# Kernel tuning notes

Hardware: AMD Instinct MI355X
Metric: run time of the kernel (lower is better)

Reference implementation:

```python
import jax, jax.numpy as jnp
import numpy as np

E = 1024
H = 16
NUM_WEIGHTS = 9


def setup_inputs() -> dict:
    key = jax.random.key(0)
    ks = jax.random.split(key, 5)
    T, B = 1024, 4
    x = jax.random.normal(ks[0], (T, B, E), dtype=jnp.float32)
    # xavier-uniform-ish init scales
    w_in = jax.random.uniform(ks[1], (NUM_WEIGHTS * E, E), dtype=jnp.float32,
                              minval=-1.0, maxval=1.0) * np.sqrt(6.0 / (NUM_WEIGHTS * E + E))
    b_in = jnp.zeros((NUM_WEIGHTS * E,), dtype=jnp.float32)
    w_out = jax.random.uniform(ks[2], (E, E), dtype=jnp.float32,
                               minval=-1.0, maxval=1.0) * np.sqrt(6.0 / (E + E))
    b_out = jnp.zeros((E,), dtype=jnp.float32)
    return {"x": x, "w_in": w_in, "b_in": b_in, "w_out": w_out, "b_out": b_out}


def _heads(t, T, B, hd):
    # [T, B, E] -> [B*H, T, hd]
    return t.reshape(T, B * H, hd).transpose(1, 0, 2)


def reference(x, w_in, b_in, w_out, b_out):
    T, B, _ = x.shape
    hd = E // H
    scaling = hd ** -0.5
    gumbel_alpha = 1.0  # const_gumbel_alpha path

    proj = jnp.einsum('tbe,fe->tbf', x, w_in) + b_in  # [T, B, 9E]
    (q, k, v, q_left, k_left, q_right, k_right,
     q_local, k_local) = jnp.split(proj, NUM_WEIGHTS, axis=-1)

    q = q * scaling
    q_local = q_local * scaling

    q, k, v = _heads(q, T, B, hd), _heads(k, T, B, hd), _heads(v, T, B, hd)
    q_left, k_left = _heads(q_left, T, B, hd), _heads(k_left, T, B, hd)
    q_right, k_right = _heads(q_right, T, B, hd), _heads(k_right, T, B, hd)
    q_local, k_local = _heads(q_local, T, B, hd), _heads(k_local, T, B, hd)

    # --- prepare_local_masking (no padding mask) ---
    left_w = jnp.einsum('btd,bsd->bts', q_left, k_left)    # [BH, T, S]
    right_w = jnp.einsum('btd,bsd->bts', q_right, k_right)
    left_sm = jax.nn.softmax(gumbel_alpha * left_w, axis=-1)
    right_sm = jax.nn.softmax(gumbel_alpha * right_w, axis=-1)

    triu = jnp.triu(jnp.ones((T, T), dtype=x.dtype))       # [S, S]
    triu_t = triu.T
    # compute_lrmask2localmask
    left_mask = left_sm @ triu
    right_mask = right_sm @ triu_t
    bw_left_mask = left_sm @ triu_t
    bw_right_mask = right_sm @ triu
    local_mask = left_mask * right_mask + bw_left_mask * bw_right_mask  # [BH, T, S]

    # --- global attention branch ---
    global_w = jnp.einsum('btd,bsd->bts', q, k)
    global_probs = jax.nn.softmax(global_w, axis=-1)

    # --- local attention branch, gated by differentiable-window mask ---
    local_w = jnp.einsum('btd,bsd->bts', q_local, k_local)
    local_sm = jax.nn.softmax(local_w, axis=-1)
    masked_local = local_sm * local_mask
    local_probs = masked_local / masked_local.sum(axis=-1, keepdims=True)

    attn_probs = 0.5 * (global_probs + local_probs)
    attn = jnp.einsum('bts,bsd->btd', attn_probs, v)        # [BH, T, hd]
    attn = attn.transpose(1, 0, 2).reshape(T, B, E)
    out = jnp.einsum('tbe,fe->tbf', attn, w_out) + b_out
    return out
```

## Files before the change

### kernel.cpp

```cpp
#include <hip/hip_runtime.h>
#include <math.h>


typedef _Float16 half8 __attribute__((ext_vector_type(8)));
typedef _Float16 half4v __attribute__((ext_vector_type(4)));
typedef _Float16 half2v __attribute__((ext_vector_type(2)));
typedef float f32x4 __attribute__((ext_vector_type(4)));

#define MFMA16(A, B, C) __builtin_amdgcn_mfma_f32_16x16x32_f16(A, B, C, 0, 0, 0)

#define SMEM_ATTN ((1088 + 10240 + 256 * 65) * 4)

static __device__ __forceinline__ unsigned packhl(_Float16 a, _Float16 b) {
  half2v v; v[0] = a; v[1] = b;
  return __builtin_bit_cast(unsigned, v);
}

__global__ __launch_bounds__(256)
void split_hl(const float* __restrict__ x, _Float16* __restrict__ xh,
              _Float16* __restrict__ xl) {
  const int i = blockIdx.x * 256 + threadIdx.x;
  const float4 v = ((const float4*)x)[i];
  half4v h, l;
  const float* f = (const float*)&v;
#pragma unroll
  for (int e = 0; e < 4; ++e) {
    h[e] = (_Float16)f[e];
    l[e] = (_Float16)(f[e] - (float)h[e]);
  }
  ((half4v*)xh)[i] = h;
  ((half4v*)xl)[i] = l;
}

template<int MODE>
__global__ __launch_bounds__(256, 2)
void gemm_mfma(const float* __restrict__ A, const float* __restrict__ B,
               const float* __restrict__ bias, float* __restrict__ C,
               _Float16* __restrict__ Ph, _Float16* __restrict__ Pl,
               const _Float16* __restrict__ Axh, const _Float16* __restrict__ Axl,
               int M, int N, int K) {
  __shared__ _Float16 Ah[128 * 64], Al[128 * 64], Bh[128 * 64], Bl[128 * 64];
  const int tid = threadIdx.x;
  const int m0 = blockIdx.x * 128, n0 = blockIdx.y * 128;
  const int wave = tid >> 6, lane = tid & 63;
  const int g2 = lane >> 4, c = lane & 15;
  const int wm = (wave >> 1) * 64, wn = (wave & 1) * 64;

  const int srow = tid >> 1;
  const int shalf = (tid & 1) * 32;
  const int swz = (srow & 7) << 3;
  const float* ap = A + (size_t)(m0 + srow) * K + shalf;
  const float* bp = B + (size_t)(n0 + srow) * K + shalf;
  const _Float16* aph = Axh + (size_t)(m0 + srow) * K + shalf;
  const _Float16* apl = Axl + (size_t)(m0 + srow) * K + shalf;

  f32x4 acc[4][4];
#pragma unroll
  for (int i = 0; i < 4; ++i)
#pragma unroll
    for (int j = 0; j < 4; ++j) acc[i][j] = (f32x4){0.f, 0.f, 0.f, 0.f};

  for (int k0 = 0; k0 < K; k0 += 64) {
    float4 av[8], bv[8];
    half8 ah8[4], al8[4];
    if (MODE == 1) {
#pragma unroll
      for (int u = 0; u < 4; ++u) {
        ah8[u] = *(const half8*)(aph + k0 + u * 8);
        al8[u] = *(const half8*)(apl + k0 + u * 8);
      }
    } else {
#pragma unroll
      for (int u = 0; u < 8; ++u) av[u] = *(const float4*)(ap + k0 + u * 4);
    }
#pragma unroll
    for (int u = 0; u < 8; ++u) bv[u] = *(const float4*)(bp + k0 + u * 4);
    __syncthreads();
    if (MODE == 1) {
#pragma unroll
      for (int u = 0; u < 4; ++u) {
        const int cc = (shalf + u * 8) ^ swz;
        *(half8*)&Ah[srow * 64 + cc] = ah8[u];
        *(half8*)&Al[srow * 64 + cc] = al8[u];
      }
    }
#pragma unroll
    for (int u = 0; u < 8; ++u) {
      const int cc = (shalf + u * 4) ^ swz;
      half4v h4b, l4b;
      const float* fb = (const float*)&bv[u];
#pragma unroll
      for (int e = 0; e < 4; ++e) {
        _Float16 hb = (_Float16)fb[e];
        h4b[e] = hb; l4b[e] = (_Float16)(fb[e] - (float)hb);
      }
      if (MODE == 0) {
        half4v h4a, l4a;
        const float* fa = (const float*)&av[u];
#pragma unroll
        for (int e = 0; e < 4; ++e) {
          _Float16 ha = (_Float16)fa[e];
          h4a[e] = ha; l4a[e] = (_Float16)(fa[e] - (float)ha);
        }
        *(half4v*)&Ah[srow * 64 + cc] = h4a;
        *(half4v*)&Al[srow * 64 + cc] = l4a;
      }
      *(half4v*)&Bh[srow * 64 + cc] = h4b;
      *(half4v*)&Bl[srow * 64 + cc] = l4b;
    }
    __syncthreads();
#pragma unroll
    for (int ks = 0; ks < 2; ++ks) {
      const int kb = ks * 32 + 8 * g2;
      half8 a_h[4], a_l[4];
#pragma unroll
      for (int i = 0; i < 4; ++i) {
        const int row = wm + i * 16 + c;
        const int cc = kb ^ ((row & 7) << 3);
        a_h[i] = *(const half8*)&Ah[row * 64 + cc];
        a_l[i] = *(const half8*)&Al[row * 64 + cc];
      }
#pragma unroll
      for (int j = 0; j < 4; ++j) {
        const int rowb = wn + j * 16 + c;
        const int cc = kb ^ ((rowb & 7) << 3);
        const half8 b_h = *(const half8*)&Bh[rowb * 64 + cc];
        const half8 b_l = *(const half8*)&Bl[rowb * 64 + cc];
#pragma unroll
        for (int i = 0; i < 4; ++i) {
          acc[i][j] = MFMA16(a_h[i], b_h, acc[i][j]);
          acc[i][j] = MFMA16(a_h[i], b_l, acc[i][j]);
          acc[i][j] = MFMA16(a_l[i], b_h, acc[i][j]);
        }
      }
    }
  }

#pragma unroll
  for (int j = 0; j < 4; ++j) {
    const int nj = n0 + wn + j * 16 + c;
    const float bz = bias[nj];
    if (MODE == 0) {
#pragma unroll
      for (int i = 0; i < 4; ++i)
#pragma unroll
        for (int q = 0; q < 4; ++q) {
          const int mi = m0 + wm + i * 16 + 4 * g2 + q;
          C[(size_t)mi * N + nj] = acc[i][j][q] + bz;
        }
    } else {
      const int w = nj >> 10, hh = (nj >> 6) & 15, d = nj & 63;
      const float scale = (w == 0 || w == 7) ? 0.125f : 1.0f;
#pragma unroll
      for (int i = 0; i < 4; ++i)
#pragma unroll
        for (int q = 0; q < 4; ++q) {
          const int mi = m0 + wm + i * 16 + 4 * g2 + q;
          const int t = mi >> 2, b2 = mi & 3;
          const size_t bb = ((size_t)w * 64 + (b2 * 16 + hh)) * 65536;
          const size_t idx = (w == 2) ? bb + (size_t)d * 1024 + t
                                      : bb + (size_t)t * 64 + d;
          const float v = (acc[i][j][q] + bz) * scale;
          const _Float16 h16 = (_Float16)v;
          Ph[idx] = h16;
          Pl[idx] = (_Float16)(v - (float)h16);
        }
    }
  }
}

__global__ __launch_bounds__(1024, 4)
void attn_mfma(const _Float16* __restrict__ Ph, const _Float16* __restrict__ Pl,
               float* __restrict__ attnOut) {
  extern __shared__ float smem[];
  float* sRed = smem;
  _Float16* sChunk = (_Float16*)(smem + 1088);
  float* sOut = smem + 1088 + 10240;
  const int flat = blockIdx.x;
  const int nf = (flat & 7) * 512 + (flat >> 3);
  const int bh = nf >> 6;
  const int t0 = (nf & 63) << 4;
  const int tid = threadIdx.x;
  const int wave = tid >> 6, lane = tid & 63;
  const int g2 = lane >> 4, c = lane & 15;
  const int sbase = wave << 6;

  auto mbase = [&](int w) { return ((size_t)w * 64 + bh) * 65536; };

  struct QF { half8 h0, h1, l0, l1; };
  auto loadQ = [&](int wq) {
    QF f;
    const _Float16* qh = Ph + mbase(wq) + (size_t)(t0 + c) * 64 + 8 * g2;
    const _Float16* ql = Pl + mbase(wq) + (size_t)(t0 + c) * 64 + 8 * g2;
    f.h0 = *(const half8*)qh; f.h1 = *(const half8*)(qh + 32);
    f.l0 = *(const half8*)ql; f.l1 = *(const half8*)(ql + 32);
    return f;
  };
  auto stileT = [&](const QF& f, const _Float16* kbh, const _Float16* kbl, int tp) {
    const int s0 = sbase + tp * 16;
    const _Float16* kh = kbh + (size_t)(s0 + c) * 64 + 8 * g2;
    const _Float16* kl = kbl + (size_t)(s0 + c) * 64 + 8 * g2;
    const half8 ah0 = *(const half8*)kh, ah1 = *(const half8*)(kh + 32);
    const half8 al0 = *(const half8*)kl, al1 = *(const half8*)(kl + 32);
    f32x4 a = {0.f, 0.f, 0.f, 0.f};
    a = MFMA16(ah0, f.h0, a);
    a = MFMA16(ah1, f.h1, a);
    a = MFMA16(ah0, f.l0, a);
    a = MFMA16(ah1, f.l1, a);
    a = MFMA16(al0, f.h0, a);
    a = MFMA16(al1, f.h1, a);
    return a;
  };

  auto put = [&](int slot, float val) {
    if (lane < 16) sRed[slot * 272 + c * 17 + wave] = val;
  };
  auto sum_pref = [&](int slot, float& pref) {
    float S = 0.f;
    pref = 0.f;
    const float* p = sRed + slot * 272 + c * 17;
#pragma unroll
    for (int w = 0; w < 16; ++w) {
      const float t = p[w];
      S += t;
      if (w < wave) pref += t;
    }
    return S;
  };
  auto sum_only = [&](int slot) {
    float S = 0.f;
    const float* p = sRed + slot * 272 + c * 17;
#pragma unroll
    for (int w = 0; w < 16; ++w) S += p[w];
    return S;
  };
  auto scan_s = [&](f32x4* v) {
    float carry = 0.f;
#pragma unroll
    for (int m = 0; m < 4; ++m) {
      v[m][1] += v[m][0];
      v[m][2] += v[m][1];
      v[m][3] += v[m][2];
      const float B = v[m][3];
      float sc = B;
      const float u1 = __shfl_up(sc, 16, 64);
      if (g2 >= 1) sc += u1;
      const float u2 = __shfl_up(sc, 32, 64);
      if (g2 >= 2) sc += u2;
      const float e = sc - B + carry;
      v[m][0] += e; v[m][1] += e; v[m][2] += e; v[m][3] += e;
      carry += __shfl(sc, 48 + c, 64);
    }
    return carry;
  };
  auto rowsum = [&](const f32x4* v) {
    float s = 0.f;
#pragma unroll
    for (int m = 0; m < 4; ++m) s += (v[m][0] + v[m][1]) + (v[m][2] + v[m][3]);
    s += __shfl_xor(s, 16, 64);
    s += __shfl_xor(s, 32, 64);
    return s;
  };

  f32x4 lv[4], rv[4];

  {
    const QF fL = loadQ(3);
    const QF fR = loadQ(5);
    const _Float16* k4h = Ph + mbase(4);
    const _Float16* k4l = Pl + mbase(4);
    const _Float16* k6h = Ph + mbase(6);
    const _Float16* k6l = Pl + mbase(6);
#pragma unroll
    for (int m = 0; m < 4; ++m) {
      lv[m] = stileT(fL, k4h, k4l, m);
      rv[m] = stileT(fR, k6h, k6l, m);
    }
#pragma unroll
    for (int m = 0; m < 4; ++m)
#pragma unroll
      for (int q = 0; q < 4; ++q) {
        lv[m][q] = __expf(lv[m][q]);
        rv[m][q] = __expf(rv[m][q]);
      }
    put(0, scan_s(lv));
    put(1, scan_s(rv));
  }
  __syncthreads();
  {
    float prefL, prefR;
    const float SL = sum_pref(0, prefL);
    const float SR = sum_pref(1, prefR);
    const float invSL = 1.f / SL, invSR = 1.f / SR;
#pragma unroll
    for (int m = 0; m < 4; ++m)
#pragma unroll
      for (int q = 0; q < 4; ++q) {
        lv[m][q] = (lv[m][q] + prefL) * invSL;
        rv[m][q] = (rv[m][q] + prefR) * invSR;
      }
    const float bL = prefL * invSL, bR = prefR * invSR;
#pragma unroll
    for (int m = 3; m >= 0; --m) {
      const float aU = __shfl_up(lv[m][3], 16, 64);
      const float bU = __shfl_up(rv[m][3], 16, 64);
      const float aM = (m > 0) ? __shfl(lv[m - 1][3], 48 + c, 64) : bL;
      const float bM = (m > 0) ? __shfl(rv[m - 1][3], 48 + c, 64) : bR;
      const float a0 = (g2 == 0) ? aM : aU;
      const float b0 = (g2 == 0) ? bM : bU;
      f32x4 nm;
      nm[0] = lv[m][0] * (1.f - b0)        + (1.f - a0)        * rv[m][0];
      nm[1] = lv[m][1] * (1.f - rv[m][0])  + (1.f - lv[m][0])  * rv[m][1];
      nm[2] = lv[m][2] * (1.f - rv[m][1])  + (1.f - lv[m][1])  * rv[m][2];
      nm[3] = lv[m][3] * (1.f - rv[m][2])  + (1.f - lv[m][2])  * rv[m][3];
      lv[m] = nm;
    }
  }
  {
    const QF fO = loadQ(7);
    const _Float16* k8h = Ph + mbase(8);
    const _Float16* k8l = Pl + mbase(8);
#pragma unroll
    for (int m = 0; m < 4; ++m) {
      const f32x4 x = stileT(fO, k8h, k8l, m);
#pragma unroll
      for (int q = 0; q < 4; ++q) rv[m][q] = __expf(x[q]) * lv[m][q];
    }
    put(2, rowsum(rv));
  }
  {
    const QF fG = loadQ(0);
    const _Float16* k1h = Ph + mbase(1);
    const _Float16* k1l = Pl + mbase(1);
#pragma unroll
    for (int m = 0; m < 4; ++m) {
      const f32x4 x = stileT(fG, k1h, k1l, m);
#pragma unroll
      for (int q = 0; q < 4; ++q) lv[m][q] = __expf(x[q]);
    }
    put(3, rowsum(lv));
  }
  __syncthreads();
  unsigned Hp[4][2], Lp[4][2];
  {
    const float scO = 0.5f / sum_only(2);
    const float scG = 0.5f / sum_only(3);
#pragma unroll
    for (int m = 0; m < 4; ++m)
#pragma unroll
      for (int p = 0; p < 2; ++p) {
        const float x0 = rv[m][2 * p] * scO + lv[m][2 * p] * scG;
        const float x1 = rv[m][2 * p + 1] * scO + lv[m][2 * p + 1] * scG;
        const _Float16 h0 = (_Float16)x0, h1 = (_Float16)x1;
        Hp[m][p] = packhl(h0, h1);
        Lp[m][p] = packhl((_Float16)(x0 - (float)h0), (_Float16)(x1 - (float)h1));
      }
  }
  f32x4 cacc[4];
#pragma unroll
  for (int dt = 0; dt < 4; ++dt) cacc[dt] = (f32x4){0.f, 0.f, 0.f, 0.f};
  {
    _Float16* chw = sChunk + wave * (2 * 16 * 40);
    const _Float16* vbh = Ph + mbase(2);
    const _Float16* vbl = Pl + mbase(2);
#pragma unroll
    for (int kk = 0; kk < 2; ++kk) {
#pragma unroll
      for (int mlo = 0; mlo < 2; ++mlo)
#pragma unroll
        for (int p = 0; p < 2; ++p) {
          const int off = c * 40 + 16 * mlo + 4 * g2 + 2 * p;
          *(unsigned*)&chw[off] = Hp[2 * kk + mlo][p];
          *(unsigned*)&chw[640 + off] = Lp[2 * kk + mlo][p];
        }
      const half8 pah = *(const half8*)&chw[c * 40 + 8 * g2];
      const half8 pal = *(const half8*)&chw[640 + c * 40 + 8 * g2];
      const int sk = sbase + kk * 32;
#pragma unroll
      for (int dt = 0; dt < 4; ++dt) {
        const _Float16* vh = vbh + (size_t)(dt * 16 + c) * 1024 + sk + 8 * g2;
        const _Float16* vl = vbl + (size_t)(dt * 16 + c) * 1024 + sk + 8 * g2;
        const half8 bh8 = *(const half8*)vh;
        const half8 bl8 = *(const half8*)vl;
        cacc[dt] = MFMA16(pah, bh8, cacc[dt]);
        cacc[dt] = MFMA16(pah, bl8, cacc[dt]);
        cacc[dt] = MFMA16(pal, bh8, cacc[dt]);
      }
    }
  }
#pragma unroll
  for (int dt = 0; dt < 4; ++dt)
#pragma unroll
    for (int q = 0; q < 4; ++q)
      sOut[(wave * 16 + 4 * g2 + q) * 65 + dt * 16 + c] = cacc[dt][q];
  __syncthreads();
  {
    const int b2 = bh >> 4, hh = bh & 15;
    const int r = tid >> 6, d = tid & 63;
    float a = 0.f;
#pragma unroll
    for (int w = 0; w < 16; ++w) a += sOut[(w * 16 + r) * 65 + d];
    attnOut[((size_t)(t0 + r) * 4 + b2) * 1024 + hh * 64 + d] = a;
  }
}

extern "C" void kernel_launch(void* const* d_in, const int* in_sizes, int n_in,
                              void* d_out, int out_size, void* d_ws, size_t ws_size,
                              hipStream_t stream) {
  const float* x     = (const float*)d_in[0];
  const float* w_in  = (const float*)d_in[1];
  const float* b_in  = (const float*)d_in[2];
  const float* w_out = (const float*)d_in[3];
  const float* b_out = (const float*)d_in[4];

  const size_t NP = (size_t)9 * 64 * 1024 * 64;
  _Float16* Ph = (_Float16*)d_ws;
  _Float16* Pl = Ph + NP;
  float* attn = (float*)(Pl + NP);
  _Float16* xh = (_Float16*)attn;
  _Float16* xl = xh + (size_t)4096 * 1024;

  (void)hipFuncSetAttribute((const void*)attn_mfma,
                            hipFuncAttributeMaxDynamicSharedMemorySize,
                            SMEM_ATTN);

  split_hl<<<4096, 256, 0, stream>>>(x, xh, xl);
  gemm_mfma<1><<<dim3(32, 72), 256, 0, stream>>>(nullptr, w_in, b_in, nullptr, Ph, Pl, xh, xl, 4096, 9216, 1024);
  attn_mfma<<<4096, 1024, SMEM_ATTN, stream>>>(Ph, Pl, attn);
  gemm_mfma<0><<<dim3(32, 8), 256, 0, stream>>>(attn, w_out, b_out, (float*)d_out, nullptr, nullptr, nullptr, nullptr, 4096, 1024, 1024);
}
```

Measured before the change: 1.051 ms.

## Tile V layout for contiguous MFMA loads and hoist global/local score MFMAs

The projection kernel now writes V in a tiled layout of 512-element blocks, one per (32-key chunk, 16-dim tile), so each lane of the attention kernel reads V as one contiguous 8-half vector. Before, each lane read 8 halves from a row strided by 1024. Separately, the QK score MFMAs for the local and global branches are moved ahead of the prefix-sum mask finalisation, so their memory loads can overlap the scan arithmetic. This costs two extra f32x4[4] register arrays per thread, which raises register pressure under launch_bounds(1024,4).

```diff
diff --git a/kernel.cpp b/kernel.cpp
--- a/kernel.cpp
+++ b/kernel.cpp
@@ -158,8 +158,13 @@
           const int mi = m0 + wm + i * 16 + 4 * g2 + q;
           const int t = mi >> 2, b2 = mi & 3;
           const size_t bb = ((size_t)w * 64 + (b2 * 16 + hh)) * 65536;
-          const size_t idx = (w == 2) ? bb + (size_t)d * 1024 + t
-                                      : bb + (size_t)t * 64 + d;
+          size_t idx;
+          if (w == 2) {
+            idx = bb + (size_t)(((t >> 6) * 2 + ((t >> 5) & 1)) * 4 + (d >> 4)) * 512
+                     + ((t >> 3) & 3) * 128 + (d & 15) * 8 + (t & 7);
+          } else {
+            idx = bb + (size_t)t * 64 + d;
+          }
           const float v = (acc[i][j][q] + bz) * scale;
           const _Float16 h16 = (_Float16)v;
           Ph[idx] = h16;
@@ -262,7 +267,7 @@
     return s;
   };
 
-  f32x4 lv[4], rv[4];
+  f32x4 lv[4], rv[4], ov[4], gv[4];
 
   {
     const QF fL = loadQ(3);
@@ -287,6 +292,19 @@
     put(1, scan_s(rv));
   }
   __syncthreads();
+  {
+    const QF fO = loadQ(7);
+    const QF fG = loadQ(0);
+    const _Float16* k8h = Ph + mbase(8);
+    const _Float16* k8l = Pl + mbase(8);
+    const _Float16* k1h = Ph + mbase(1);
+    const _Float16* k1l = Pl + mbase(1);
+#pragma unroll
+    for (int m = 0; m < 4; ++m) {
+      ov[m] = stileT(fO, k8h, k8l, m);
+      gv[m] = stileT(fG, k1h, k1l, m);
+    }
+  }
   {
     float prefL, prefR;
     const float SL = sum_pref(0, prefL);
@@ -317,28 +335,15 @@
     }
   }
   {
-    const QF fO = loadQ(7);
-    const _Float16* k8h = Ph + mbase(8);
-    const _Float16* k8l = Pl + mbase(8);
-#pragma unroll
-    for (int m = 0; m < 4; ++m) {
-      const f32x4 x = stileT(fO, k8h, k8l, m);
-#pragma unroll
-      for (int q = 0; q < 4; ++q) rv[m][q] = __expf(x[q]) * lv[m][q];
-    }
-    put(2, rowsum(rv));
-  }
-  {
-    const QF fG = loadQ(0);
-    const _Float16* k1h = Ph + mbase(1);
-    const _Float16* k1l = Pl + mbase(1);
-#pragma unroll
-    for (int m = 0; m < 4; ++m) {
-      const f32x4 x = stileT(fG, k1h, k1l, m);
-#pragma unroll
-      for (int q = 0; q < 4; ++q) lv[m][q] = __expf(x[q]);
-    }
-    put(3, rowsum(lv));
+#pragma unroll
+    for (int m = 0; m < 4; ++m)
+#pragma unroll
+      for (int q = 0; q < 4; ++q) {
+        ov[m][q] = __expf(ov[m][q]) * lv[m][q];
+        gv[m][q] = __expf(gv[m][q]);
+      }
+    put(2, rowsum(ov));
+    put(3, rowsum(gv));
   }
   __syncthreads();
   unsigned Hp[4][2], Lp[4][2];
@@ -349,8 +354,8 @@
     for (int m = 0; m < 4; ++m)
 #pragma unroll
       for (int p = 0; p < 2; ++p) {
-        const float x0 = rv[m][2 * p] * scO + lv[m][2 * p] * scG;
-        const float x1 = rv[m][2 * p + 1] * scO + lv[m][2 * p + 1] * scG;
+        const float x0 = ov[m][2 * p] * scO + gv[m][2 * p] * scG;
+        const float x1 = ov[m][2 * p + 1] * scO + gv[m][2 * p + 1] * scG;
         const _Float16 h0 = (_Float16)x0, h1 = (_Float16)x1;
         Hp[m][p] = packhl(h0, h1);
         Lp[m][p] = packhl((_Float16)(x0 - (float)h0), (_Float16)(x1 - (float)h1));
@@ -375,13 +380,11 @@
         }
       const half8 pah = *(const half8*)&chw[c * 40 + 8 * g2];
       const half8 pal = *(const half8*)&chw[640 + c * 40 + 8 * g2];
-      const int sk = sbase + kk * 32;
 #pragma unroll
       for (int dt = 0; dt < 4; ++dt) {
-        const _Float16* vh = vbh + (size_t)(dt * 16 + c) * 1024 + sk + 8 * g2;
-        const _Float16* vl = vbl + (size_t)(dt * 16 + c) * 1024 + sk + 8 * g2;
-        const half8 bh8 = *(const half8*)vh;
-        const half8 bl8 = *(const half8*)vl;
+        const size_t vo = (size_t)(((wave * 2 + kk) * 4 + dt) << 9) + (g2 << 7) + (c << 3);
+        const half8 bh8 = *(const half8*)(vbh + vo);
+        const half8 bl8 = *(const half8*)(vbl + vo);
         cacc[dt] = MFMA16(pah, bh8, cacc[dt]);
         cacc[dt] = MFMA16(pah, bl8, cacc[dt]);
         cacc[dt] = MFMA16(pal, bh8, cacc[dt]);
```

New measurement: 968.1 us. 1.09x faster.
